# Kernel tuning notes

Hardware: AMD Instinct MI355X
Metric: run time of the kernel (lower is better)

Reference implementation:

```python
import jax, jax.numpy as jnp
import numpy as np

NUM_ITER = 10
H, W = 1024, 1024


def _conv(x, w, pad):
    # NCHW cross-correlation, matching torch.nn.Conv2d
    return jax.lax.conv_general_dilated(
        x, w, window_strides=(1, 1), padding=pad,
        dimension_numbers=("NCHW", "OIHW", "NCHW"))


def setup_inputs() -> dict:
    key = jax.random.key(0)
    x = jax.random.normal(key, (1, 2, H, W), dtype=jnp.float32)
    gx = jnp.array([[1.0, 0.0, -1.0], [2.0, 0.0, -2.0], [1.0, 0.0, -1.0]], dtype=jnp.float32)
    gy = jnp.array([[1.0, 2.0, 1.0], [0.0, 0.0, 0.0], [-1.0, -2.0, -1.0]], dtype=jnp.float32)
    grad_w = jnp.stack([gx, gy])[:, None]  # [2,1,3,3] frozen Sobel-like gradient filters
    wx = jnp.array([[1.0, 1.0]], dtype=jnp.float32)        # divergence-x weights [1,2]
    wy = jnp.array([[1.0], [1.0]], dtype=jnp.float32)      # divergence-y weights [2,1]
    lambda_ = jnp.array([0.15], dtype=jnp.float32)
    tau = jnp.array([0.25], dtype=jnp.float32)
    theta = jnp.array([0.3], dtype=jnp.float32)
    return {"x": x, "grad_w": grad_w, "wx": wx, "wy": wy,
            "lambda_": lambda_, "tau": tau, "theta": theta}


def _forward(x, grad_w, wx, wy, lambda_, tau, theta):
    _, _, h, w = x.shape  # x: [1, 2 frames, H, W]
    x1 = x[:, 1:]                       # [1,1,H,W] second frame
    rho_c = x1 - x[:, :-1]              # [1,1,H,W] temporal difference
    grad_im = _conv(x1, grad_w, ((1, 1), (1, 1)))            # [1,2,H,W]
    norm_grad = jnp.sum(grad_im * grad_im, axis=1, keepdims=True)  # [1,1,H,W]
    wx_k = wx.reshape(1, 1, 1, 2)
    wy_k = wy.reshape(1, 1, 2, 1)
    tl = theta * lambda_                # [1]
    r = tau / theta                     # [1]
    u0 = jnp.zeros((1, 2, h, w), x.dtype)
    p0 = jnp.zeros((2, 2, h, w), x.dtype)

    def body(carry, _):
        u, p = carry
        rho = rho_c + jnp.sum(grad_im * u, axis=1, keepdims=True)  # [1,1,H,W]
        th = tl * norm_grad
        a = jnp.abs(rho)
        v = (u
             - (a < th).astype(u.dtype) * rho * grad_im / norm_grad
             - (a > th).astype(u.dtype) * tl * grad_im * jnp.sign(rho))  # [1,2,H,W]
        # divergence: depthwise 1x2 / 2x1 stencils on the two dual channels
        div_x = _conv(p[0][:, None], wx_k, ((0, 0), (1, 0)))[:, 0]  # [2,H,W]
        div_y = _conv(p[1][:, None], wy_k, ((1, 0), (0, 0)))[:, 0]  # [2,H,W]
        u = v + theta * (div_x + div_y)                             # [1,2,H,W]
        # per-flow-channel spatial gradient -> [2 flow, 2 dirs, H, W]
        gradu = _conv(u.reshape(2, 1, h, w), grad_w, ((1, 1), (1, 1)))
        p = (p + r * gradu) / (1.0 + r * jnp.sum(jnp.abs(gradu)))
        return (u, p), None

    (u, _), _ = jax.lax.scan(body, (u0, p0), None, length=NUM_ITER)
    return u


def reference(x, grad_w, wx, wy, lambda_, tau, theta):
    return _forward(x, grad_w, wx, wy, lambda_, tau, theta)
```

## Files before the change

### kernel.cpp

```cpp
#include <hip/hip_runtime.h>

typedef unsigned long long ull;

#define HH 1024
#define WW 1024
#define HWSZ (HH * WW)
#define NV (HWSZ / 4)
#define NITER 10
#define NB 256
#define BT 512

__device__ __forceinline__ float fald(const float* p) {
    return __hip_atomic_load(p, __ATOMIC_RELAXED, __HIP_MEMORY_SCOPE_AGENT);
}
__device__ __forceinline__ float2 ald2(const float* p) {
    ull v = __hip_atomic_load((const ull*)p, __ATOMIC_RELAXED, __HIP_MEMORY_SCOPE_AGENT);
    return __builtin_bit_cast(float2, v);
}
__device__ __forceinline__ void ast2(float* p, float a, float b) {
    float2 f; f.x = a; f.y = b;
    __hip_atomic_store((ull*)p, __builtin_bit_cast(ull, f),
                       __ATOMIC_RELAXED, __HIP_MEMORY_SCOPE_AGENT);
}
__device__ __forceinline__ unsigned uald(const unsigned* p) {
    return __hip_atomic_load(p, __ATOMIC_RELAXED, __HIP_MEMORY_SCOPE_AGENT);
}
__device__ __forceinline__ void uast(unsigned* p, unsigned v) {
    __hip_atomic_store(p, v, __ATOMIC_RELAXED, __HIP_MEMORY_SCOPE_AGENT);
}
__device__ __forceinline__ unsigned uaadd(unsigned* p, unsigned v) {
    return __hip_atomic_fetch_add(p, v, __ATOMIC_RELAXED, __HIP_MEMORY_SCOPE_AGENT);
}
__device__ __forceinline__ void faadd(float* p, float v) {
    __hip_atomic_fetch_add(p, v, __ATOMIC_RELAXED, __HIP_MEMORY_SCOPE_AGENT);
}
__device__ __forceinline__ void vm0() { asm volatile("s_waitcnt vmcnt(0)" ::: "memory"); }
__device__ __forceinline__ void waitflag(const unsigned* p) {
    while (uald(p) == 0u) __builtin_amdgcn_s_sleep(1);
}

__device__ __forceinline__ int FU(int t, int bt)  { return (t * NB + bt) * 16; }
__device__ __forceinline__ int FP(int t, int bt)  { return 40960 + (t * NB + bt) * 16; }
__device__ __forceinline__ int SGC(int t, int g)  { return 81920 + (t * 16 + g) * 16; }
__device__ __forceinline__ int SC(int t)          { return 84480 + t * 16; }
__device__ __forceinline__ int SD(int t, int g)   { return 84640 + (t * 16 + g) * 16; }
__device__ __forceinline__ int SGA(int t, int g)  { return 87200 + (t * 16 + g) * 16; }
__device__ __forceinline__ int SA(int t)          { return 89760 + t * 16; }

__device__ __forceinline__ size_t UEX(int par, int bt, int side, int ch) {
    return ((size_t)(((par * NB + bt) * 2 + side) * 2 + ch)) * 1024;
}
__device__ __forceinline__ size_t PEX(int bt, int pl) {
    return (size_t)(bt * 2 + pl) * 1024;
}

__device__ __forceinline__ void row6(const float* __restrict__ pl, int h, int w0, float a[6]) {
    if ((unsigned)h < (unsigned)HH) {
        const float* rp = pl + h * WW + w0;
        const float4 v = *(const float4*)rp;
        a[0] = (w0 > 0) ? rp[-1] : 0.0f;
        a[1] = v.x; a[2] = v.y; a[3] = v.z; a[4] = v.w;
        a[5] = (w0 + 4 < WW) ? rp[4] : 0.0f;
    } else {
        a[0] = a[1] = a[2] = a[3] = a[4] = a[5] = 0.0f;
    }
}
__device__ __forceinline__ void row6lds(const float* rp, int w0, float a[6]) {
    a[0] = (w0 > 0) ? rp[w0 - 1] : 0.0f;
    const float4 v = *(const float4*)(rp + w0);
    a[1] = v.x; a[2] = v.y; a[3] = v.z; a[4] = v.w;
    a[5] = (w0 + 4 < WW) ? rp[w0 + 4] : 0.0f;
}
__device__ __forceinline__ void halo6(const float* rb, int w0, float a[6]) {
    float2 p1 = ald2(rb + w0), p2 = ald2(rb + w0 + 2);
    a[1] = p1.x; a[2] = p1.y; a[3] = p2.x; a[4] = p2.y;
    a[0] = (w0 > 0) ? ald2(rb + w0 - 2).y : 0.0f;
    a[5] = (w0 + 4 < WW) ? ald2(rb + w0 + 4).x : 0.0f;
}

__device__ __forceinline__ float cgx(const float t[6], const float m[6], const float b[6], int i) {
    return (t[i] - t[i + 2]) + 2.0f * (m[i] - m[i + 2]) + (b[i] - b[i + 2]);
}
__device__ __forceinline__ float cgy(const float t[6], const float b[6], int i) {
    return (t[i] + 2.0f * t[i + 1] + t[i + 2]) - (b[i] + 2.0f * b[i + 1] + b[i + 2]);
}
__device__ __forceinline__ void grad4(const float T[6], const float M[6], const float B[6],
                                      float gx[4], float gy[4], float& acc) {
    #pragma unroll
    for (int i = 0; i < 4; ++i) {
        gx[i] = cgx(T, M, B, i);
        gy[i] = cgy(T, B, i);
        acc += fabsf(gx[i]) + fabsf(gy[i]);
    }
}

__device__ __forceinline__ float2 vupd(float rc, float g0, float g1,
                                       float u0, float u1, float tl) {
    float ng = g0 * g0 + g1 * g1;
    float rho = rc + g0 * u0 + g1 * u1;
    float a = fabsf(rho);
    float th = tl * ng;
    float sgn = (rho > 0.0f) ? 1.0f : ((rho < 0.0f) ? -1.0f : 0.0f);
    float d0 = 0.0f, d1 = 0.0f;
    if (a < th)      { float s = rho / ng; d0 = s * g0; d1 = s * g1; }
    else if (a > th) { d0 = tl * g0 * sgn; d1 = tl * g1 * sgn; }
    return make_float2(u0 - d0, u1 - d1);
}

__global__ __launch_bounds__(256) void k_zero(float* __restrict__ f) {
    const float4 z = make_float4(0.f, 0.f, 0.f, 0.f);
    ((float4*)f)[blockIdx.x * 256 + threadIdx.x] = z;
}

__global__ __launch_bounds__(512, 1) void k_tvl1(
    const float* __restrict__ x,
    const float* __restrict__ wxp, const float* __restrict__ wyp,
    const float* __restrict__ lamp, const float* __restrict__ taup,
    const float* __restrict__ thetap,
    float* __restrict__ ug,
    float* __restrict__ uex,
    float* __restrict__ pex,
    unsigned* __restrict__ F)
{
    float* Ff = (float*)F;
    const int tid  = threadIdx.x;
    const int s    = tid >> 8;
    const int stid = tid & 255;
    const int b    = blockIdx.x;
    const int bt   = ((b & 7) << 5) + (b >> 3);
    const int g    = bt >> 4;
    const int hb   = bt << 2;
    const int w0   = stid << 2;

    __shared__ float sm[4][2][1024];
    __shared__ float lshp[8][257];
    __shared__ float pnx[2][1024];
    __shared__ float red[8];
    __shared__ float sS;

    const float theta = thetap[0];
    const float tl    = theta * lamp[0];
    const float r     = taup[0] / theta;
    const float wx0 = wxp[0], wx1 = wxp[1];
    const float wy0 = wyp[0], wy1 = wyp[1];

    float rc[2][4], g0[2][4], g1[2][4], u0[2][4], u1[2][4];
    float pn00[2][4], pn01[2][4], pn10[2][4], pn11[2][4];

    {
        const float* x1p = x + HWSZ;
        #pragma unroll
        for (int rr = 0; rr < 2; ++rr) {
            const int h = hb + 2 * s + rr;
            float t6[6], m6[6], b6[6];
            row6(x1p, h - 1, w0, t6);
            row6(x1p, h,     w0, m6);
            row6(x1p, h + 1, w0, b6);
            const float4 x0v = *(const float4*)(x + h * WW + w0);
            const float x0a[4] = {x0v.x, x0v.y, x0v.z, x0v.w};
            #pragma unroll
            for (int i = 0; i < 4; ++i) {
                g0[rr][i] = cgx(t6, m6, b6, i);
                g1[rr][i] = cgy(t6, b6, i);
                rc[rr][i] = m6[i + 1] - x0a[i];
                u0[rr][i] = u1[rr][i] = 0.0f;
                pn00[rr][i] = pn01[rr][i] = pn10[rr][i] = pn11[rr][i] = 0.0f;
            }
        }
    }

    float inv = 1.0f;
    #pragma unroll 1
    for (int t = 0; t < NITER; ++t) {
        const int par = t & 1;

        float2 vv[2][4];
        #pragma unroll
        for (int rr = 0; rr < 2; ++rr)
            #pragma unroll
            for (int i = 0; i < 4; ++i)
                vv[rr][i] = vupd(rc[rr][i], g0[rr][i], g1[rr][i], u0[rr][i], u1[rr][i], tl);
        #pragma unroll
        for (int rr = 0; rr < 2; ++rr) {
            lshp[(s * 2 + rr) * 2 + 0][stid] = pn00[rr][3];
            lshp[(s * 2 + rr) * 2 + 1][stid] = pn01[rr][3];
        }
        if (s == 0) {
            #pragma unroll
            for (int i = 0; i < 4; ++i) {
                pnx[0][w0 + i] = pn10[1][i];
                pnx[1][w0 + i] = pn11[1][i];
            }
        }
        if (t > 0) {
            if (tid == 0) {
                waitflag(F + SD(t - 1, g));
                sS = fald(Ff + SA(t - 1));
            }
            if (tid == 64 && bt > 0)
                waitflag(F + FP(t - 1, bt - 1));
        }
        __syncthreads();
        if (t > 0) inv = 1.0f / (1.0f + r * sS);

        float l00[2], l01[2];
        #pragma unroll
        for (int rr = 0; rr < 2; ++rr) {
            l00[rr] = stid ? lshp[(s * 2 + rr) * 2 + 0][stid - 1] : 0.f;
            l01[rr] = stid ? lshp[(s * 2 + rr) * 2 + 1][stid - 1] : 0.f;
        }
        float up10[2][4], up11[2][4];
        if (s == 0) {
            if (t > 0 && bt > 0) {
                const float* p0 = pex + PEX(bt - 1, 0) + w0;
                const float* p1 = pex + PEX(bt - 1, 1) + w0;
                float2 a0 = ald2(p0), a1 = ald2(p0 + 2);
                float2 c0 = ald2(p1), c1 = ald2(p1 + 2);
                up10[0][0] = a0.x; up10[0][1] = a0.y; up10[0][2] = a1.x; up10[0][3] = a1.y;
                up11[0][0] = c0.x; up11[0][1] = c0.y; up11[0][2] = c1.x; up11[0][3] = c1.y;
            } else {
                #pragma unroll
                for (int i = 0; i < 4; ++i) { up10[0][i] = 0.f; up11[0][i] = 0.f; }
            }
        } else {
            #pragma unroll
            for (int i = 0; i < 4; ++i) { up10[0][i] = pnx[0][w0 + i]; up11[0][i] = pnx[1][w0 + i]; }
        }
        #pragma unroll
        for (int i = 0; i < 4; ++i) { up10[1][i] = pn10[0][i]; up11[1][i] = pn11[0][i]; }

        #pragma unroll
        for (int rr = 0; rr < 2; ++rr)
            #pragma unroll
            for (int i = 0; i < 4; ++i) {
                const float pl00 = i ? pn00[rr][i - 1] : l00[rr];
                const float pl01 = i ? pn01[rr][i - 1] : l01[rr];
                const float dx0 = (wx1 * pn00[rr][i] + wx0 * pl00) * inv;
                const float dx1 = (wx1 * pn01[rr][i] + wx0 * pl01) * inv;
                const float dy0 = (wy1 * pn10[rr][i] + wy0 * up10[rr][i]) * inv;
                const float dy1 = (wy1 * pn11[rr][i] + wy0 * up11[rr][i]) * inv;
                u0[rr][i] = vv[rr][i].x + theta * (dx0 + dy0);
                u1[rr][i] = vv[rr][i].y + theta * (dx1 + dy1);
            }

        if (t == NITER - 1) {
            #pragma unroll
            for (int rr = 0; rr < 2; ++rr) {
                const int h = hb + 2 * s + rr;
                *(float4*)(ug + h * WW + w0) =
                    make_float4(u0[rr][0], u0[rr][1], u0[rr][2], u0[rr][3]);
                *(float4*)(ug + HWSZ + h * WW + w0) =
                    make_float4(u1[rr][0], u1[rr][1], u1[rr][2], u1[rr][3]);
            }
            break;
        }
        {
            const int rr = (s == 0) ? 0 : 1;
            float* e0 = uex + UEX(par, bt, s, 0) + w0;
            float* e1 = uex + UEX(par, bt, s, 1) + w0;
            ast2(e0,     u0[rr][0], u0[rr][1]); ast2(e0 + 2, u0[rr][2], u0[rr][3]);
            ast2(e1,     u1[rr][0], u1[rr][1]); ast2(e1 + 2, u1[rr][2], u1[rr][3]);
        }
        vm0();
        __syncthreads();
        if (tid == 0) uast(F + FU(t, bt), 1u);

        #pragma unroll
        for (int rr = 0; rr < 2; ++rr) {
            const int q = 2 * s + rr;
            *(float4*)&sm[q][0][w0] = make_float4(u0[rr][0], u0[rr][1], u0[rr][2], u0[rr][3]);
            *(float4*)&sm[q][1][w0] = make_float4(u1[rr][0], u1[rr][1], u1[rr][2], u1[rr][3]);
        }
        if (tid == 0   && bt > 0)      waitflag(F + FU(t, bt - 1));
        if (tid == 256 && bt < NB - 1) waitflag(F + FU(t, bt + 1));
        __syncthreads();

        float GT[2][6];
        {
            const bool have = (s == 0) ? (bt > 0) : (bt < NB - 1);
            if (have) {
                const int nbt  = (s == 0) ? bt - 1 : bt + 1;
                const int side = (s == 0) ? 1 : 0;
                halo6(uex + UEX(par, nbt, side, 0), w0, GT[0]);
                halo6(uex + UEX(par, nbt, side, 1), w0, GT[1]);
            } else {
                #pragma unroll
                for (int i = 0; i < 6; ++i) { GT[0][i] = 0.f; GT[1][i] = 0.f; }
            }
        }
        float Wm[3][2][6];
        #pragma unroll
        for (int j = 0; j < 3; ++j)
            #pragma unroll
            for (int c = 0; c < 2; ++c)
                row6lds(&sm[s + j][c][0], w0, Wm[j][c]);

        float gx[2][2][4], gy[2][2][4];
        float local = 0.0f;
        if (s == 0) {
            #pragma unroll
            for (int c = 0; c < 2; ++c) {
                grad4(GT[c],    Wm[0][c], Wm[1][c], gx[0][c], gy[0][c], local);
                grad4(Wm[0][c], Wm[1][c], Wm[2][c], gx[1][c], gy[1][c], local);
            }
        } else {
            #pragma unroll
            for (int c = 0; c < 2; ++c) {
                grad4(Wm[0][c], Wm[1][c], Wm[2][c], gx[0][c], gy[0][c], local);
                grad4(Wm[1][c], Wm[2][c], GT[c],    gx[1][c], gy[1][c], local);
            }
        }
        float sr = local;
        #pragma unroll
        for (int off = 32; off > 0; off >>= 1) sr += __shfl_down(sr, off, 64);
        if ((tid & 63) == 0) red[tid >> 6] = sr;

        #pragma unroll
        for (int rr = 0; rr < 2; ++rr)
            #pragma unroll
            for (int i = 0; i < 4; ++i) {
                pn00[rr][i] = pn00[rr][i] * inv + r * gx[rr][0][i];
                pn01[rr][i] = pn01[rr][i] * inv + r * gy[rr][0][i];
                pn10[rr][i] = pn10[rr][i] * inv + r * gx[rr][1][i];
                pn11[rr][i] = pn11[rr][i] * inv + r * gy[rr][1][i];
            }
        if (s == 1) {
            float* e0 = pex + PEX(bt, 0) + w0;
            float* e1 = pex + PEX(bt, 1) + w0;
            ast2(e0,     pn10[1][0], pn10[1][1]); ast2(e0 + 2, pn10[1][2], pn10[1][3]);
            ast2(e1,     pn11[1][0], pn11[1][1]); ast2(e1 + 2, pn11[1][2], pn11[1][3]);
        }
        vm0();
        __syncthreads();
        if (tid == 0) {
            uast(F + FP(t, bt), 1u);
            float sblock = red[0] + red[1] + red[2] + red[3]
                         + red[4] + red[5] + red[6] + red[7];
            faadd(Ff + SGA(t, g), sblock);
            vm0();
            if (uaadd(F + SGC(t, g), 1u) == 15u) {
                float gsum = fald(Ff + SGA(t, g));
                faadd(Ff + SA(t), gsum);
                vm0();
                if (uaadd(F + SC(t), 1u) == 15u) {
                    #pragma unroll
                    for (int j = 0; j < 16; ++j) uast(F + SD(t, j), 1u);
                }
            }
        }
    }
}

__global__ __launch_bounds__(256) void fb_pre(float* __restrict__ u, float* __restrict__ pn) {
    int v = blockIdx.x * 256 + threadIdx.x;
    int idx = v * 4;
    float4 z = make_float4(0.f, 0.f, 0.f, 0.f);
    *(float4*)(u + idx) = z;
    *(float4*)(u + HWSZ + idx) = z;
    *(float4*)(pn + idx) = z;
    *(float4*)(pn + HWSZ + idx) = z;
    *(float4*)(pn + 2 * HWSZ + idx) = z;
    *(float4*)(pn + 3 * HWSZ + idx) = z;
}

__device__ __forceinline__ float fb_inv(const float* __restrict__ SbF, int t, float r,
                                        float* red, int tid) {
    if (t == 0) return 1.0f;
    const float4 pv = ((const float4*)(SbF + ((t - 1) & 1) * 1024))[tid];
    float s = pv.x + pv.y + pv.z + pv.w;
    #pragma unroll
    for (int off = 32; off > 0; off >>= 1) s += __shfl_down(s, off, 64);
    if ((tid & 63) == 0) red[tid >> 6] = s;
    __syncthreads();
    return 1.0f / (1.0f + r * (red[0] + red[1] + red[2] + red[3]));
}

__global__ __launch_bounds__(256) void fb_u(const float* __restrict__ x,
                                            const float* __restrict__ wxp,
                                            const float* __restrict__ wyp,
                                            const float* __restrict__ lamp,
                                            const float* __restrict__ taup,
                                            const float* __restrict__ thetap,
                                            float* __restrict__ u,
                                            const float* __restrict__ pn,
                                            const float* __restrict__ SbF, int t) {
    __shared__ float red[4];
    int tid = threadIdx.x;
    float theta = thetap[0];
    float tl = theta * lamp[0];
    float r = taup[0] / theta;
    float inv = fb_inv(SbF, t, r, red, tid);

    int v = blockIdx.x * 256 + tid;
    int idx = v * 4;
    int h = idx >> 10, w0 = idx & (WW - 1);
    const float* x1p = x + HWSZ;
    float t6[6], m6[6], b6[6];
    row6(x1p, h - 1, w0, t6);
    row6(x1p, h,     w0, m6);
    row6(x1p, h + 1, w0, b6);
    const float4 x0v = *(const float4*)(x + idx);
    const float x0a[4] = {x0v.x, x0v.y, x0v.z, x0v.w};

    const float wx0 = wxp[0], wx1 = wxp[1];
    const float wy0 = wyp[0], wy1 = wyp[1];
    const float* pn00 = pn;
    const float* pn01 = pn + HWSZ;
    const float* pn10 = pn + 2 * HWSZ;
    const float* pn11 = pn + 3 * HWSZ;
    float4 a00v = *(const float4*)(pn00 + idx);
    float4 a01v = *(const float4*)(pn01 + idx);
    float4 a10v = *(const float4*)(pn10 + idx);
    float4 a11v = *(const float4*)(pn11 + idx);
    const float a00[4] = {a00v.x, a00v.y, a00v.z, a00v.w};
    const float a01[4] = {a01v.x, a01v.y, a01v.z, a01v.w};
    const float a10[4] = {a10v.x, a10v.y, a10v.z, a10v.w};
    const float a11[4] = {a11v.x, a11v.y, a11v.z, a11v.w};
    float a00l = (w0 > 0) ? pn00[idx - 1] : 0.f;
    float a01l = (w0 > 0) ? pn01[idx - 1] : 0.f;
    float4 z4 = make_float4(0.f, 0.f, 0.f, 0.f);
    float4 q10 = (h > 0) ? *(const float4*)(pn10 + idx - WW) : z4;
    float4 q11 = (h > 0) ? *(const float4*)(pn11 + idx - WW) : z4;
    const float up10[4] = {q10.x, q10.y, q10.z, q10.w};
    const float up11[4] = {q11.x, q11.y, q11.z, q11.w};
    float4 u0v = *(const float4*)(u + idx);
    float4 u1v = *(const float4*)(u + HWSZ + idx);
    const float u0a[4] = {u0v.x, u0v.y, u0v.z, u0v.w};
    const float u1a[4] = {u1v.x, u1v.y, u1v.z, u1v.w};

    float o0[4], o1[4];
    #pragma unroll
    for (int i = 0; i < 4; ++i) {
        float g0i = cgx(t6, m6, b6, i);
        float g1i = cgy(t6, b6, i);
        float rci = m6[i + 1] - x0a[i];
        float2 vvv = vupd(rci, g0i, g1i, u0a[i], u1a[i], tl);
        float pl00 = i ? a00[i - 1] : a00l;
        float pl01 = i ? a01[i - 1] : a01l;
        float dx0 = (wx1 * a00[i] + wx0 * pl00) * inv;
        float dx1 = (wx1 * a01[i] + wx0 * pl01) * inv;
        float dy0 = (wy1 * a10[i] + wy0 * up10[i]) * inv;
        float dy1 = (wy1 * a11[i] + wy0 * up11[i]) * inv;
        o0[i] = vvv.x + theta * (dx0 + dy0);
        o1[i] = vvv.y + theta * (dx1 + dy1);
    }
    *(float4*)(u + idx)        = make_float4(o0[0], o0[1], o0[2], o0[3]);
    *(float4*)(u + HWSZ + idx) = make_float4(o1[0], o1[1], o1[2], o1[3]);
}

__global__ __launch_bounds__(256) void fb_pn(const float* __restrict__ taup,
                                             const float* __restrict__ thetap,
                                             const float* __restrict__ u,
                                             float* __restrict__ pn,
                                             float* __restrict__ SbF, int t) {
    __shared__ float red[4];
    int tid = threadIdx.x;
    float r = taup[0] / thetap[0];
    float inv = fb_inv(SbF, t, r, red, tid);

    int v = blockIdx.x * 256 + tid;
    int idx = v * 4;
    int h = idx >> 10, w0 = idx & (WW - 1);
    float tA[6], mA[6], bA[6], tB[6], mB[6], bB[6];
    row6(u,        h - 1, w0, tA);
    row6(u,        h,     w0, mA);
    row6(u,        h + 1, w0, bA);
    row6(u + HWSZ, h - 1, w0, tB);
    row6(u + HWSZ, h,     w0, mB);
    row6(u + HWSZ, h + 1, w0, bB);

    float gx0[4], gy0[4], gx1[4], gy1[4];
    float local = 0.0f;
    #pragma unroll
    for (int i = 0; i < 4; ++i) {
        gx0[i] = cgx(tA, mA, bA, i);
        gy0[i] = cgy(tA, bA, i);
        gx1[i] = cgx(tB, mB, bB, i);
        gy1[i] = cgy(tB, bB, i);
        local += fabsf(gx0[i]) + fabsf(gy0[i]) + fabsf(gx1[i]) + fabsf(gy1[i]);
    }
    float s = local;
    #pragma unroll
    for (int off = 32; off > 0; off >>= 1) s += __shfl_down(s, off, 64);
    if ((tid & 63) == 0) red[tid >> 6] = s;
    __syncthreads();
    if (tid == 0) SbF[(t & 1) * 1024 + blockIdx.x] = red[0] + red[1] + red[2] + red[3];

    float* pn00 = pn;
    float* pn01 = pn + HWSZ;
    float* pn10 = pn + 2 * HWSZ;
    float* pn11 = pn + 3 * HWSZ;
    float4 q0 = *(const float4*)(pn00 + idx);
    float4 q1 = *(const float4*)(pn01 + idx);
    float4 q2 = *(const float4*)(pn10 + idx);
    float4 q3 = *(const float4*)(pn11 + idx);
    *(float4*)(pn00 + idx) = make_float4(q0.x * inv + r * gx0[0], q0.y * inv + r * gx0[1],
                                         q0.z * inv + r * gx0[2], q0.w * inv + r * gx0[3]);
    *(float4*)(pn01 + idx) = make_float4(q1.x * inv + r * gy0[0], q1.y * inv + r * gy0[1],
                                         q1.z * inv + r * gy0[2], q1.w * inv + r * gy0[3]);
    *(float4*)(pn10 + idx) = make_float4(q2.x * inv + r * gx1[0], q2.y * inv + r * gx1[1],
                                         q2.z * inv + r * gx1[2], q2.w * inv + r * gx1[3]);
    *(float4*)(pn11 + idx) = make_float4(q3.x * inv + r * gy1[0], q3.y * inv + r * gy1[1],
                                         q3.z * inv + r * gy1[2], q3.w * inv + r * gy1[3]);
}

extern "C" void kernel_launch(void* const* d_in, const int* in_sizes, int n_in,
                              void* d_out, int out_size, void* d_ws, size_t ws_size,
                              hipStream_t stream) {
    const float* x     = (const float*)d_in[0];
    const float* wx    = (const float*)d_in[2];
    const float* wy    = (const float*)d_in[3];
    const float* lam   = (const float*)d_in[4];
    const float* tau   = (const float*)d_in[5];
    const float* theta = (const float*)d_in[6];

    float* ug = (float*)d_out;
    float* ws = (float*)d_ws;

    float*    uex = ws;
    float*    pex = ws + (size_t)2097152;
    unsigned* F   = (unsigned*)(ws + (size_t)2097152 + 524288);

    k_zero<<<dim3(88), dim3(256), 0, stream>>>((float*)F);

    void* args[] = {(void*)&x, (void*)&wx, (void*)&wy, (void*)&lam, (void*)&tau,
                    (void*)&theta, (void*)&ug, (void*)&uex, (void*)&pex, (void*)&F};
    hipError_t err = hipLaunchCooperativeKernel((const void*)k_tvl1, dim3(NB), dim3(BT),
                                                args, 0, stream);
    if (err != hipSuccess) {
        (void)hipGetLastError();
        float* pn  = ws;
        float* SbF = ws + 4 * (size_t)HWSZ;
        dim3 block(256), gridV(NV / 256);
        fb_pre<<<gridV, block, 0, stream>>>(ug, pn);
        for (int t = 0; t < NITER; ++t) {
            fb_u<<<gridV, block, 0, stream>>>(x, wx, wy, lam, tau, theta, ug, pn, SbF, t);
            fb_pn<<<gridV, block, 0, stream>>>(tau, theta, ug, pn, SbF, t);
        }
    }
}
```

Baseline: 187.5 us.

## Defer global-sum wait, pack the sum into the done flag, use shuffle halos

The wait on the per-iteration global abs-gradient sum moves to after the divergence terms are computed, so that work overlaps the cross-block reduction latency. The last reducer now writes the negated total sum into the done flags, so waiters read the value straight from the flag instead of doing a separate atomic load. Stencil edge values come from neighbouring lanes via wavefront shuffles instead of extra LDS and global loads, and the pnx LDS accesses become float4. The cost is an extra __syncthreads per iteration, and correctness depends on the flag encoding never being zero.

```diff
diff --git a/kernel.cpp b/kernel.cpp
--- a/kernel.cpp
+++ b/kernel.cpp
@@ -65,17 +65,23 @@
         a[0] = a[1] = a[2] = a[3] = a[4] = a[5] = 0.0f;
     }
 }
-__device__ __forceinline__ void row6lds(const float* rp, int w0, float a[6]) {
-    a[0] = (w0 > 0) ? rp[w0 - 1] : 0.0f;
+__device__ __forceinline__ void row6sh(const float* rp, int w0, int lane, float a[6]) {
     const float4 v = *(const float4*)(rp + w0);
     a[1] = v.x; a[2] = v.y; a[3] = v.z; a[4] = v.w;
-    a[5] = (w0 + 4 < WW) ? rp[w0 + 4] : 0.0f;
-}
-__device__ __forceinline__ void halo6(const float* rb, int w0, float a[6]) {
+    float lft = __shfl_up(v.w, 1, 64);
+    float rgt = __shfl_down(v.x, 1, 64);
+    if (lane == 0)  lft = (w0 > 0) ? rp[w0 - 1] : 0.0f;
+    if (lane == 63) rgt = (w0 + 4 < WW) ? rp[w0 + 4] : 0.0f;
+    a[0] = lft; a[5] = rgt;
+}
+__device__ __forceinline__ void halo6sh(const float* rb, int w0, int lane, float a[6]) {
     float2 p1 = ald2(rb + w0), p2 = ald2(rb + w0 + 2);
     a[1] = p1.x; a[2] = p1.y; a[3] = p2.x; a[4] = p2.y;
-    a[0] = (w0 > 0) ? ald2(rb + w0 - 2).y : 0.0f;
-    a[5] = (w0 + 4 < WW) ? ald2(rb + w0 + 4).x : 0.0f;
+    float lft = __shfl_up(p2.y, 1, 64);
+    float rgt = __shfl_down(p1.x, 1, 64);
+    if (lane == 0)  lft = (w0 > 0) ? fald(rb + w0 - 1) : 0.0f;
+    if (lane == 63) rgt = (w0 + 4 < WW) ? fald(rb + w0 + 4) : 0.0f;
+    a[0] = lft; a[5] = rgt;
 }
 
 __device__ __forceinline__ float cgx(const float t[6], const float m[6], const float b[6], int i) {
@@ -126,6 +132,7 @@
     const int tid  = threadIdx.x;
     const int s    = tid >> 8;
     const int stid = tid & 255;
+    const int lane = tid & 63;
     const int b    = blockIdx.x;
     const int bt   = ((b & 7) << 5) + (b >> 3);
     const int g    = bt >> 4;
@@ -186,22 +193,12 @@
             lshp[(s * 2 + rr) * 2 + 1][stid] = pn01[rr][3];
         }
         if (s == 0) {
-            #pragma unroll
-            for (int i = 0; i < 4; ++i) {
-                pnx[0][w0 + i] = pn10[1][i];
-                pnx[1][w0 + i] = pn11[1][i];
-            }
-        }
-        if (t > 0) {
-            if (tid == 0) {
-                waitflag(F + SD(t - 1, g));
-                sS = fald(Ff + SA(t - 1));
-            }
-            if (tid == 64 && bt > 0)
-                waitflag(F + FP(t - 1, bt - 1));
-        }
+            *(float4*)&pnx[0][w0] = make_float4(pn10[1][0], pn10[1][1], pn10[1][2], pn10[1][3]);
+            *(float4*)&pnx[1][w0] = make_float4(pn11[1][0], pn11[1][1], pn11[1][2], pn11[1][3]);
+        }
+        if (t > 0 && tid == 64 && bt > 0)
+            waitflag(F + FP(t - 1, bt - 1));
         __syncthreads();
-        if (t > 0) inv = 1.0f / (1.0f + r * sS);
 
         float l00[2], l01[2];
         #pragma unroll
@@ -223,24 +220,41 @@
                 for (int i = 0; i < 4; ++i) { up10[0][i] = 0.f; up11[0][i] = 0.f; }
             }
         } else {
-            #pragma unroll
-            for (int i = 0; i < 4; ++i) { up10[0][i] = pnx[0][w0 + i]; up11[0][i] = pnx[1][w0 + i]; }
+            float4 q0 = *(const float4*)&pnx[0][w0];
+            float4 q1 = *(const float4*)&pnx[1][w0];
+            up10[0][0] = q0.x; up10[0][1] = q0.y; up10[0][2] = q0.z; up10[0][3] = q0.w;
+            up11[0][0] = q1.x; up11[0][1] = q1.y; up11[0][2] = q1.z; up11[0][3] = q1.w;
         }
         #pragma unroll
         for (int i = 0; i < 4; ++i) { up10[1][i] = pn10[0][i]; up11[1][i] = pn11[0][i]; }
 
+        float ws0[2][4], ws1[2][4];
         #pragma unroll
         for (int rr = 0; rr < 2; ++rr)
             #pragma unroll
             for (int i = 0; i < 4; ++i) {
                 const float pl00 = i ? pn00[rr][i - 1] : l00[rr];
                 const float pl01 = i ? pn01[rr][i - 1] : l01[rr];
-                const float dx0 = (wx1 * pn00[rr][i] + wx0 * pl00) * inv;
-                const float dx1 = (wx1 * pn01[rr][i] + wx0 * pl01) * inv;
-                const float dy0 = (wy1 * pn10[rr][i] + wy0 * up10[rr][i]) * inv;
-                const float dy1 = (wy1 * pn11[rr][i] + wy0 * up11[rr][i]) * inv;
-                u0[rr][i] = vv[rr][i].x + theta * (dx0 + dy0);
-                u1[rr][i] = vv[rr][i].y + theta * (dx1 + dy1);
+                ws0[rr][i] = theta * ((wx1 * pn00[rr][i] + wx0 * pl00)
+                                    + (wy1 * pn10[rr][i] + wy0 * up10[rr][i]));
+                ws1[rr][i] = theta * ((wx1 * pn01[rr][i] + wx0 * pl01)
+                                    + (wy1 * pn11[rr][i] + wy0 * up11[rr][i]));
+            }
+        if (t > 0) {
+            if (tid == 0) {
+                unsigned v;
+                while ((v = uald(F + SD(t - 1, g))) == 0u) __builtin_amdgcn_s_sleep(1);
+                sS = -__uint_as_float(v);
+            }
+            __syncthreads();
+            inv = 1.0f / (1.0f + r * sS);
+        }
+        #pragma unroll
+        for (int rr = 0; rr < 2; ++rr)
+            #pragma unroll
+            for (int i = 0; i < 4; ++i) {
+                u0[rr][i] = vv[rr][i].x + inv * ws0[rr][i];
+                u1[rr][i] = vv[rr][i].y + inv * ws1[rr][i];
             }
 
         if (t == NITER - 1) {
@@ -281,8 +295,8 @@
             if (have) {
                 const int nbt  = (s == 0) ? bt - 1 : bt + 1;
                 const int side = (s == 0) ? 1 : 0;
-                halo6(uex + UEX(par, nbt, side, 0), w0, GT[0]);
-                halo6(uex + UEX(par, nbt, side, 1), w0, GT[1]);
+                halo6sh(uex + UEX(par, nbt, side, 0), w0, lane, GT[0]);
+                halo6sh(uex + UEX(par, nbt, side, 1), w0, lane, GT[1]);
             } else {
                 #pragma unroll
                 for (int i = 0; i < 6; ++i) { GT[0][i] = 0.f; GT[1][i] = 0.f; }
@@ -293,7 +307,7 @@
         for (int j = 0; j < 3; ++j)
             #pragma unroll
             for (int c = 0; c < 2; ++c)
-                row6lds(&sm[s + j][c][0], w0, Wm[j][c]);
+                row6sh(&sm[s + j][c][0], w0, lane, Wm[j][c]);
 
         float gx[2][2][4], gy[2][2][4];
         float local = 0.0f;
@@ -343,8 +357,10 @@
                 faadd(Ff + SA(t), gsum);
                 vm0();
                 if (uaadd(F + SC(t), 1u) == 15u) {
+                    float tot = fald(Ff + SA(t));
+                    unsigned enc = __float_as_uint(-tot);
                     #pragma unroll
-                    for (int j = 0; j < 16; ++j) uast(F + SD(t, j), 1u);
+                    for (int j = 0; j < 16; ++j) uast(F + SD(t, j), enc);
                 }
             }
         }
```

New measurement: 179.3 us. 1.05x faster.
